# Performance work log

Measured on AMD Instinct MI355X. Metric: run time of the kernel, lower is better.

Reference implementation:

```python
import jax, jax.numpy as jnp
from jax import lax
import numpy as np


def setup_inputs() -> dict:
    key = jax.random.key(0)
    ks = jax.random.split(key, 10)
    B, C, T, H, W = 4, 128, 32, 24, 24
    M, k_t, k_s, mix_k = 3, 3, 3, 3
    s = 0.05
    q = jax.random.normal(ks[0], (B, C, T, H, W), jnp.float32)
    k = jax.random.normal(ks[1], (B, C, T, H, W), jnp.float32)
    v = jax.random.normal(ks[2], (B, C, T, H, W), jnp.float32)
    # depthwise 3D kernel banks: [M, C, 1, k_t, k_s, k_s] (OIDHW per branch, groups=C)
    Wk = jax.random.normal(ks[3], (M, C, 1, k_t, k_s, k_s), jnp.float32) * s
    Wv = jax.random.normal(ks[4], (M, C, 1, k_t, k_s, k_s), jnp.float32) * s
    # mix predictor: 1x1 conv1d (pointwise) + causal conv1d C->M
    pre_w = jax.random.normal(ks[5], (C, C), jnp.float32) * s
    pre_b = jax.random.normal(ks[6], (C,), jnp.float32) * s
    mix_w = jax.random.normal(ks[7], (M, C, mix_k), jnp.float32) * s
    mix_b = jax.random.normal(ks[8], (M,), jnp.float32) * s
    return {"q": q, "k": k, "v": v, "Wk": Wk, "Wv": Wv,
            "pre_w": pre_w, "pre_b": pre_b, "mix_w": mix_w, "mix_b": mix_b}


def _mix_alpha(q, pre_w, pre_b, mix_w, mix_b):
    # q: [B,C,T,H,W] -> global spatial pool -> [B,C,T]
    qg = q.mean(axis=(3, 4))
    h = jnp.einsum('oc,bct->bot', pre_w, qg) + pre_b[None, :, None]
    h = jax.nn.gelu(h, approximate=False)  # torch nn.GELU default = exact
    mix_k = mix_w.shape[-1]
    logits = lax.conv_general_dilated(
        h, mix_w, window_strides=(1,), padding=[(mix_k - 1, 0)],
        dimension_numbers=('NCH', 'OIH', 'NCH')) + mix_b[None, :, None]
    return jax.nn.softmax(logits, axis=1)  # [B,M,T]


def _dwconv3d_causal(x, w):
    # x: [B,C,T,H,W], w: [C,1,k_t,k_h,k_w] depthwise (groups=C)
    C = x.shape[1]
    k_t, k_h, k_w = w.shape[2], w.shape[3], w.shape[4]
    pad = [(k_t - 1, 0), (k_h // 2, k_h // 2), (k_w // 2, k_w // 2)]
    return lax.conv_general_dilated(
        x, w, window_strides=(1, 1, 1), padding=pad,
        dimension_numbers=('NCDHW', 'OIDHW', 'NCDHW'),
        feature_group_count=C)


def reference(q, k, v, Wk, Wv, pre_w, pre_b, mix_w, mix_b):
    alpha = _mix_alpha(q, pre_w, pre_b, mix_w, mix_b)  # [B,M,T]
    # all M depthwise branches at once: [M,B,C,T,H,W]
    km = jax.vmap(_dwconv3d_causal, in_axes=(None, 0))(k, Wk)
    vm = jax.vmap(_dwconv3d_causal, in_axes=(None, 0))(v, Wv)
    # per-time mixture-weighted sum over M
    k_out = jnp.einsum('mbcthw,bmt->bcthw', km, alpha)
    v_out = jnp.einsum('mbcthw,bmt->bcthw', vm, alpha)
    return (k_out, v_out)
```

## Files before the change

### kernel.cpp

```cpp
#include <hip/hip_runtime.h>
#include <math.h>

namespace {
constexpr int Bn = 4, Cn = 128, Tn = 32, Hn = 24, Wn = 24, Mn = 3;
constexpr int HWn = Hn * Wn;
constexpr int TTile = 8;
constexpr int PL = TTile + 2;
constexpr int RS = 28;
constexpr int PS = 26 * RS;
}

__global__ __launch_bounds__(256) void pool_kernel(const float* __restrict__ q,
                                                   float* __restrict__ qg) {
    int wave = threadIdx.x >> 6;
    int lane = threadIdx.x & 63;
    int plane = blockIdx.x * 4 + wave;
    const float4* p = (const float4*)(q + (size_t)plane * HWn);
    float4 a = p[lane];
    float4 b = p[lane + 64];
    float s = (a.x + a.y) + (a.z + a.w) + (b.x + b.y) + (b.z + b.w);
    if (lane < 16) {
        float4 c = p[128 + lane];
        s += (c.x + c.y) + (c.z + c.w);
    }
#pragma unroll
    for (int off = 32; off > 0; off >>= 1) s += __shfl_down(s, off);
    if (lane == 0) qg[plane] = s * (1.0f / 576.0f);
}

__global__ __launch_bounds__(512) void alpha_kernel(const float* __restrict__ qg,
                                                    const float* __restrict__ pre_w,
                                                    const float* __restrict__ pre_b,
                                                    const float* __restrict__ mix_w,
                                                    const float* __restrict__ mix_b,
                                                    float* __restrict__ alpha) {
    __shared__ float qg_s[Cn * Tn];
    __shared__ float h_s[Cn * (Tn + 2)];
    __shared__ float mw_s[Mn * Cn * 3];
    __shared__ float l_s[Mn * Tn];
    int b = blockIdx.x;
    int tid = threadIdx.x;
    for (int i = tid; i < Cn * Tn; i += 512) qg_s[i] = qg[b * Cn * Tn + i];
    for (int i = tid; i < Mn * Cn * 3; i += 512) mw_s[i] = mix_w[i];
    __syncthreads();
    {
        int o = tid >> 2;
        int t0 = (tid & 3) * 8;
        float bias = pre_b[o];
        float acc[8];
#pragma unroll
        for (int j = 0; j < 8; ++j) acc[j] = 0.f;
        const float* wrow = pre_w + o * Cn;
#pragma unroll 2
        for (int cb = 0; cb < Cn; cb += 8) {
            float wv[8];
#pragma unroll
            for (int j = 0; j < 8; ++j) wv[j] = wrow[cb + j];
#pragma unroll
            for (int j = 0; j < 8; ++j)
#pragma unroll
                for (int i = 0; i < 8; ++i)
                    acc[i] += wv[j] * qg_s[(cb + j) * Tn + t0 + i];
        }
        if ((tid & 3) == 0) { h_s[o * (Tn + 2) + 0] = 0.f; h_s[o * (Tn + 2) + 1] = 0.f; }
#pragma unroll
        for (int j = 0; j < 8; ++j) {
            float x = acc[j] + bias;
            h_s[o * (Tn + 2) + 2 + t0 + j] = 0.5f * x * (1.0f + erff(x * 0.70710678118654752f));
        }
    }
    __syncthreads();
    if (tid < Mn * Tn) {
        int m = tid / Tn, t = tid % Tn;
        float acc = mix_b[m];
#pragma unroll 8
        for (int c = 0; c < Cn; ++c) {
            const float* mw = mw_s + (m * Cn + c) * 3;
            const float* hp = h_s + c * (Tn + 2) + t;
            acc += mw[0] * hp[0] + mw[1] * hp[1] + mw[2] * hp[2];
        }
        l_s[m * Tn + t] = acc;
    }
    __syncthreads();
    if (tid < Tn) {
        int t = tid;
        float l0 = l_s[t], l1 = l_s[Tn + t], l2 = l_s[2 * Tn + t];
        float mx = fmaxf(l0, fmaxf(l1, l2));
        float e0 = expf(l0 - mx), e1 = expf(l1 - mx), e2 = expf(l2 - mx);
        float inv = 1.0f / (e0 + e1 + e2);
        alpha[(b * Mn + 0) * Tn + t] = e0 * inv;
        alpha[(b * Mn + 1) * Tn + t] = e1 * inv;
        alpha[(b * Mn + 2) * Tn + t] = e2 * inv;
    }
}

__global__ __launch_bounds__(384) void conv_kernel(const float* __restrict__ kin,
                                                   const float* __restrict__ vin,
                                                   const float* __restrict__ Wk,
                                                   const float* __restrict__ Wv,
                                                   const float* __restrict__ alpha,
                                                   float* __restrict__ out) {
    __shared__ float s[PL * PS];
    __shared__ float sw[TTile * 27];

    int bid = blockIdx.x;
    int tt = bid & 3;
    int c  = (bid >> 2) & 127;
    int b  = (bid >> 9) & 3;
    int br = bid >> 11;
    int t0 = tt * TTile;
    int tid = threadIdx.x;
    const size_t plane_base = (size_t)(b * Cn + c) * Tn;
    const float* __restrict__ src = br ? vin : kin;
    const float* __restrict__ Wb  = br ? Wv : Wk;

    float4 z4 = make_float4(0.f, 0.f, 0.f, 0.f);
    for (int i = tid; i < PL * PS / 4; i += 384) ((float4*)s)[i] = z4;
    __syncthreads();

    for (int idx = tid; idx < PL * 144; idx += 384) {
        int p = idx / 144;
        int cell = idx - p * 144;
        int r = cell / 6;
        int c4 = cell - r * 6;
        int tp = t0 - 2 + p;
        if (tp >= 0) {
            float4 val = *(const float4*)(src + (plane_base + tp) * HWn + r * 24 + c4 * 4);
            float* dst = s + p * PS + (r + 1) * RS + 1 + c4 * 4;
            dst[0] = val.x; dst[1] = val.y; dst[2] = val.z; dst[3] = val.w;
        }
    }
    if (tid < TTile * 27) {
        int tl = tid / 27;
        int widx = tid - tl * 27;
        float a0 = alpha[(b * Mn + 0) * Tn + t0 + tl];
        float a1 = alpha[(b * Mn + 1) * Tn + t0 + tl];
        float a2 = alpha[(b * Mn + 2) * Tn + t0 + tl];
        sw[tid] = a0 * Wb[(0 * Cn + c) * 27 + widx]
                + a1 * Wb[(1 * Cn + c) * 27 + widx]
                + a2 * Wb[(2 * Cn + c) * 27 + widx];
    }
    __syncthreads();

    int tl = tid / 48;
    int rem = tid - tl * 48;
    int h = rem >> 1;
    int w0 = (rem & 1) * 12;
    const float* wp = sw + tl * 27;
    float acc[12];
#pragma unroll
    for (int j = 0; j < 12; ++j) acc[j] = 0.f;
#pragma unroll
    for (int dt = 0; dt < 3; ++dt) {
#pragma unroll
        for (int dh = 0; dh < 3; ++dh) {
            const float* rp = s + (tl + dt) * PS + (h + dh) * RS + w0;
            float bf[14];
#pragma unroll
            for (int j = 0; j < 14; ++j) bf[j] = rp[j];
#pragma unroll
            for (int dw = 0; dw < 3; ++dw) {
                float wc = wp[dt * 9 + dh * 3 + dw];
#pragma unroll
                for (int j = 0; j < 12; ++j) acc[j] += bf[j + dw] * wc;
            }
        }
    }
    size_t obase = (plane_base + t0 + tl) * HWn + h * Wn + w0;
    float* op = out + (br ? (size_t)Bn * Cn * Tn * HWn : 0) + obase;
#pragma unroll
    for (int j = 0; j < 3; ++j)
        ((float4*)op)[j] = make_float4(acc[4*j], acc[4*j+1], acc[4*j+2], acc[4*j+3]);
}

extern "C" void kernel_launch(void* const* d_in, const int* in_sizes, int n_in,
                              void* d_out, int out_size, void* d_ws, size_t ws_size,
                              hipStream_t stream) {
    const float* q     = (const float*)d_in[0];
    const float* k     = (const float*)d_in[1];
    const float* v     = (const float*)d_in[2];
    const float* Wk    = (const float*)d_in[3];
    const float* Wv    = (const float*)d_in[4];
    const float* pre_w = (const float*)d_in[5];
    const float* pre_b = (const float*)d_in[6];
    const float* mix_w = (const float*)d_in[7];
    const float* mix_b = (const float*)d_in[8];
    float* out = (float*)d_out;

    float* qg    = (float*)d_ws;
    float* alpha = qg + Bn * Cn * Tn;

    hipLaunchKernelGGL(pool_kernel, dim3(Bn * Cn * Tn / 4), dim3(256), 0, stream, q, qg);
    hipLaunchKernelGGL(alpha_kernel, dim3(Bn), dim3(512), 0, stream,
                       qg, pre_w, pre_b, mix_w, mix_b, alpha);
    hipLaunchKernelGGL(conv_kernel, dim3(2 * Bn * Cn * (Tn / TTile)), dim3(384), 0, stream,
                       k, v, Wk, Wv, alpha, out);
}
```

Baseline: 215.0 us.

## Register-block two output rows per thread in conv and vectorize LDS reads

The depthwise conv kernel now has each thread compute two adjacent output rows of 12 pixels. Each loaded 16-float LDS row segment, read as float4, feeds both accumulators, so LDS traffic per output drops and the block shrinks to 192 threads. Building the mixed weights now overlaps with the shared-memory zero fill, ahead of the first barrier. The alpha kernel's pointwise matmul is also re-tiled to 2 outputs by 4 timesteps per thread with float4 loads. The cost is more registers per thread and fewer threads per block, which may lower occupancy or latency hiding.

```diff
diff --git a/kernel.cpp b/kernel.cpp
--- a/kernel.cpp
+++ b/kernel.cpp
@@ -7,7 +7,7 @@
 constexpr int TTile = 8;
 constexpr int PL = TTile + 2;
 constexpr int RS = 28;
-constexpr int PS = 26 * RS;
+constexpr int PSr = 26 * RS;
 }
 
 __global__ __launch_bounds__(256) void pool_kernel(const float* __restrict__ q,
@@ -40,33 +40,48 @@
     __shared__ float l_s[Mn * Tn];
     int b = blockIdx.x;
     int tid = threadIdx.x;
-    for (int i = tid; i < Cn * Tn; i += 512) qg_s[i] = qg[b * Cn * Tn + i];
+    for (int i = tid; i < Cn * Tn / 4; i += 512)
+        ((float4*)qg_s)[i] = ((const float4*)(qg + b * Cn * Tn))[i];
     for (int i = tid; i < Mn * Cn * 3; i += 512) mw_s[i] = mix_w[i];
     __syncthreads();
     {
-        int o = tid >> 2;
-        int t0 = (tid & 3) * 8;
-        float bias = pre_b[o];
-        float acc[8];
-#pragma unroll
-        for (int j = 0; j < 8; ++j) acc[j] = 0.f;
-        const float* wrow = pre_w + o * Cn;
-#pragma unroll 2
-        for (int cb = 0; cb < Cn; cb += 8) {
-            float wv[8];
-#pragma unroll
-            for (int j = 0; j < 8; ++j) wv[j] = wrow[cb + j];
-#pragma unroll
-            for (int j = 0; j < 8; ++j)
-#pragma unroll
-                for (int i = 0; i < 8; ++i)
-                    acc[i] += wv[j] * qg_s[(cb + j) * Tn + t0 + i];
-        }
-        if ((tid & 3) == 0) { h_s[o * (Tn + 2) + 0] = 0.f; h_s[o * (Tn + 2) + 1] = 0.f; }
-#pragma unroll
-        for (int j = 0; j < 8; ++j) {
-            float x = acc[j] + bias;
-            h_s[o * (Tn + 2) + 2 + t0 + j] = 0.5f * x * (1.0f + erff(x * 0.70710678118654752f));
+        int o0 = (tid >> 3) * 2;
+        int t0 = (tid & 7) * 4;
+        float acc0[4] = {0.f, 0.f, 0.f, 0.f};
+        float acc1[4] = {0.f, 0.f, 0.f, 0.f};
+        const float* w0r = pre_w + (size_t)o0 * Cn;
+        const float* w1r = w0r + Cn;
+#pragma unroll 4
+        for (int cb = 0; cb < Cn; cb += 4) {
+            float4 wa = *(const float4*)(w0r + cb);
+            float4 wb = *(const float4*)(w1r + cb);
+            float w0v[4] = {wa.x, wa.y, wa.z, wa.w};
+            float w1v[4] = {wb.x, wb.y, wb.z, wb.w};
+            float4 g[4];
+#pragma unroll
+            for (int j = 0; j < 4; ++j)
+                g[j] = *(const float4*)(qg_s + (cb + j) * Tn + t0);
+#pragma unroll
+            for (int j = 0; j < 4; ++j) {
+                acc0[0] += w0v[j] * g[j].x; acc0[1] += w0v[j] * g[j].y;
+                acc0[2] += w0v[j] * g[j].z; acc0[3] += w0v[j] * g[j].w;
+                acc1[0] += w1v[j] * g[j].x; acc1[1] += w1v[j] * g[j].y;
+                acc1[2] += w1v[j] * g[j].z; acc1[3] += w1v[j] * g[j].w;
+            }
+        }
+        float b0 = pre_b[o0], b1 = pre_b[o0 + 1];
+        if (t0 == 0) {
+            h_s[o0 * (Tn + 2) + 0] = 0.f; h_s[o0 * (Tn + 2) + 1] = 0.f;
+            h_s[(o0 + 1) * (Tn + 2) + 0] = 0.f; h_s[(o0 + 1) * (Tn + 2) + 1] = 0.f;
+        }
+#pragma unroll
+        for (int j = 0; j < 4; ++j) {
+            float x0 = acc0[j] + b0;
+            float x1 = acc1[j] + b1;
+            h_s[o0 * (Tn + 2) + 2 + t0 + j] =
+                0.5f * x0 * (1.0f + erff(x0 * 0.70710678118654752f));
+            h_s[(o0 + 1) * (Tn + 2) + 2 + t0 + j] =
+                0.5f * x1 * (1.0f + erff(x1 * 0.70710678118654752f));
         }
     }
     __syncthreads();
@@ -94,13 +109,13 @@
     }
 }
 
-__global__ __launch_bounds__(384) void conv_kernel(const float* __restrict__ kin,
+__global__ __launch_bounds__(192) void conv_kernel(const float* __restrict__ kin,
                                                    const float* __restrict__ vin,
                                                    const float* __restrict__ Wk,
                                                    const float* __restrict__ Wv,
                                                    const float* __restrict__ alpha,
                                                    float* __restrict__ out) {
-    __shared__ float s[PL * PS];
+    __shared__ float s[PL * PSr];
     __shared__ float sw[TTile * 27];
 
     int bid = blockIdx.x;
@@ -115,10 +130,20 @@
     const float* __restrict__ Wb  = br ? Wv : Wk;
 
     float4 z4 = make_float4(0.f, 0.f, 0.f, 0.f);
-    for (int i = tid; i < PL * PS / 4; i += 384) ((float4*)s)[i] = z4;
-    __syncthreads();
-
-    for (int idx = tid; idx < PL * 144; idx += 384) {
+    for (int i = tid; i < PL * PSr / 4; i += 192) ((float4*)s)[i] = z4;
+    for (int i = tid; i < TTile * 27; i += 192) {
+        int tl = i / 27;
+        int widx = i - tl * 27;
+        float a0 = alpha[(b * Mn + 0) * Tn + t0 + tl];
+        float a1 = alpha[(b * Mn + 1) * Tn + t0 + tl];
+        float a2 = alpha[(b * Mn + 2) * Tn + t0 + tl];
+        sw[i] = a0 * Wb[(0 * Cn + c) * 27 + widx]
+              + a1 * Wb[(1 * Cn + c) * 27 + widx]
+              + a2 * Wb[(2 * Cn + c) * 27 + widx];
+    }
+    __syncthreads();
+
+    for (int idx = tid; idx < PL * 144; idx += 192) {
         int p = idx / 144;
         int cell = idx - p * 144;
         int r = cell / 6;
@@ -126,51 +151,57 @@
         int tp = t0 - 2 + p;
         if (tp >= 0) {
             float4 val = *(const float4*)(src + (plane_base + tp) * HWn + r * 24 + c4 * 4);
-            float* dst = s + p * PS + (r + 1) * RS + 1 + c4 * 4;
+            float* dst = s + p * PSr + (r + 1) * RS + 1 + c4 * 4;
             dst[0] = val.x; dst[1] = val.y; dst[2] = val.z; dst[3] = val.w;
         }
     }
-    if (tid < TTile * 27) {
-        int tl = tid / 27;
-        int widx = tid - tl * 27;
-        float a0 = alpha[(b * Mn + 0) * Tn + t0 + tl];
-        float a1 = alpha[(b * Mn + 1) * Tn + t0 + tl];
-        float a2 = alpha[(b * Mn + 2) * Tn + t0 + tl];
-        sw[tid] = a0 * Wb[(0 * Cn + c) * 27 + widx]
-                + a1 * Wb[(1 * Cn + c) * 27 + widx]
-                + a2 * Wb[(2 * Cn + c) * 27 + widx];
-    }
-    __syncthreads();
-
-    int tl = tid / 48;
-    int rem = tid - tl * 48;
-    int h = rem >> 1;
-    int w0 = (rem & 1) * 12;
+    __syncthreads();
+
+    int tl = tid / 24;
+    int rem = tid - tl * 24;
+    int h2 = rem >> 1;
+    int wseg = rem & 1;
+    int h0 = h2 * 2;
+    int w0 = wseg * 12;
     const float* wp = sw + tl * 27;
-    float acc[12];
-#pragma unroll
-    for (int j = 0; j < 12; ++j) acc[j] = 0.f;
+    float acc0[12], acc1[12];
+#pragma unroll
+    for (int j = 0; j < 12; ++j) { acc0[j] = 0.f; acc1[j] = 0.f; }
 #pragma unroll
     for (int dt = 0; dt < 3; ++dt) {
-#pragma unroll
-        for (int dh = 0; dh < 3; ++dh) {
-            const float* rp = s + (tl + dt) * PS + (h + dh) * RS + w0;
-            float bf[14];
-#pragma unroll
-            for (int j = 0; j < 14; ++j) bf[j] = rp[j];
-#pragma unroll
-            for (int dw = 0; dw < 3; ++dw) {
-                float wc = wp[dt * 9 + dh * 3 + dw];
-#pragma unroll
-                for (int j = 0; j < 12; ++j) acc[j] += bf[j + dw] * wc;
+        const float* w9 = wp + dt * 9;
+        const float* pb = s + (tl + dt) * PSr + h0 * RS + w0;
+#pragma unroll
+        for (int j = 0; j < 4; ++j) {
+            const float4* rp = (const float4*)(pb + j * RS);
+            float4 f0 = rp[0], f1 = rp[1], f2 = rp[2], f3 = rp[3];
+            float f[16] = {f0.x, f0.y, f0.z, f0.w, f1.x, f1.y, f1.z, f1.w,
+                           f2.x, f2.y, f2.z, f2.w, f3.x, f3.y, f3.z, f3.w};
+            if (j <= 2) {
+#pragma unroll
+                for (int dw = 0; dw < 3; ++dw) {
+                    float wc = w9[j * 3 + dw];
+#pragma unroll
+                    for (int i = 0; i < 12; ++i) acc0[i] += f[i + dw] * wc;
+                }
             }
-        }
-    }
-    size_t obase = (plane_base + t0 + tl) * HWn + h * Wn + w0;
+            if (j >= 1) {
+#pragma unroll
+                for (int dw = 0; dw < 3; ++dw) {
+                    float wc = w9[(j - 1) * 3 + dw];
+#pragma unroll
+                    for (int i = 0; i < 12; ++i) acc1[i] += f[i + dw] * wc;
+                }
+            }
+        }
+    }
+    size_t obase = (plane_base + t0 + tl) * HWn + h0 * Wn + w0;
     float* op = out + (br ? (size_t)Bn * Cn * Tn * HWn : 0) + obase;
 #pragma unroll
-    for (int j = 0; j < 3; ++j)
-        ((float4*)op)[j] = make_float4(acc[4*j], acc[4*j+1], acc[4*j+2], acc[4*j+3]);
+    for (int j = 0; j < 3; ++j) {
+        ((float4*)op)[j] = make_float4(acc0[4*j], acc0[4*j+1], acc0[4*j+2], acc0[4*j+3]);
+        ((float4*)(op + Wn))[j] = make_float4(acc1[4*j], acc1[4*j+1], acc1[4*j+2], acc1[4*j+3]);
+    }
 }
 
 extern "C" void kernel_launch(void* const* d_in, const int* in_sizes, int n_in,
@@ -193,6 +224,6 @@
     hipLaunchKernelGGL(pool_kernel, dim3(Bn * Cn * Tn / 4), dim3(256), 0, stream, q, qg);
     hipLaunchKernelGGL(alpha_kernel, dim3(Bn), dim3(512), 0, stream,
                        qg, pre_w, pre_b, mix_w, mix_b, alpha);
-    hipLaunchKernelGGL(conv_kernel, dim3(2 * Bn * Cn * (Tn / TTile)), dim3(384), 0, stream,
+    hipLaunchKernelGGL(conv_kernel, dim3(2 * Bn * Cn * (Tn / TTile)), dim3(192), 0, stream,
                        k, v, Wk, Wv, alpha, out);
 }
```

Result: slower. 222.4 us (+3.5%).
